# Kernel optimization log

Hardware: AMD Instinct MI355X
Metric: run time of the kernel (lower is better)

The kernel has to match this reference:

```python
import jax, jax.numpy as jnp
import numpy as np

N, M, D = 16384, 16384, 3


def setup_inputs() -> dict:
    key = jax.random.key(0)
    kx, ky = jax.random.split(key)
    x = jax.random.normal(kx, (N, D), dtype=jnp.float32)
    y = jax.random.normal(ky, (M, D), dtype=jnp.float32)
    return {"x": x, "y": y}


def reference(x, y):
    # One-sided Chamfer: for each x_i, min_j ||y_j - x_i||^2.
    x2 = jnp.sum(x * x, axis=-1)                       # [N]
    y2 = jnp.sum(y * y, axis=-1)                       # [M]
    d2 = x2[:, None] - 2.0 * (x @ y.T) + y2[None, :]   # [N, M] pairwise sq dists
    closest_dists = jnp.min(d2, axis=1)                # [N]
    return jnp.sum(closest_dists), closest_dists
```

## Files before the change

### kernel.cpp

```cpp
#include <hip/hip_runtime.h>


constexpr int TPB = 256;
constexpr int XPT = 8;
constexpr int MAX_YCHUNK = 512;

__global__ __launch_bounds__(TPB) void chamfer_main(
    const float* __restrict__ x, const float* __restrict__ y,
    float* __restrict__ part, int N, int M, int ychunk) {
  __shared__ float4 sy[MAX_YCHUNK];
  const int t = threadIdx.x;
  const int bx = blockIdx.x;
  const int s = blockIdx.y;

  for (int jj = t; jj < ychunk; jj += TPB) {
    const int j = s * ychunk + jj;
    if (j < M) {
      const float y0 = y[3 * j], y1 = y[3 * j + 1], y2 = y[3 * j + 2];
      sy[jj] = make_float4(-2.0f * y0, -2.0f * y1, -2.0f * y2,
                           y0 * y0 + y1 * y1 + y2 * y2);
    } else {
      sy[jj] = make_float4(0.0f, 0.0f, 0.0f, __builtin_inff());
    }
  }
  __syncthreads();

  float x0[XPT], x1[XPT], x2[XPT], mn[XPT];
#pragma unroll
  for (int k = 0; k < XPT; k++) {
    const int i = bx * (TPB * XPT) + k * TPB + t;
    const int ic = (i < N) ? i : 0;
    x0[k] = x[3 * ic];
    x1[k] = x[3 * ic + 1];
    x2[k] = x[3 * ic + 2];
    mn[k] = __builtin_inff();
  }

#pragma unroll 4
  for (int jj = 0; jj < ychunk; jj++) {
    const float4 q = sy[jj];
#pragma unroll
    for (int k = 0; k < XPT; k++) {
      mn[k] = fminf(mn[k],
                    fmaf(x0[k], q.x, fmaf(x1[k], q.y, fmaf(x2[k], q.z, q.w))));
    }
  }

#pragma unroll
  for (int k = 0; k < XPT; k++) {
    const int i = bx * (TPB * XPT) + k * TPB + t;
    if (i < N) part[(size_t)s * N + i] = mn[k];
  }
}

__global__ __launch_bounds__(TPB) void chamfer_reduce(
    const float* __restrict__ x, const float* __restrict__ part,
    float* __restrict__ out, int N, int S) {
  const int t = threadIdx.x;
  const int i = blockIdx.x * TPB + t;

  float d = 0.0f;
  if (i < N) {
    float m = __builtin_inff();
#pragma unroll 8
    for (int s = 0; s < S; s++) m = fminf(m, part[(size_t)s * N + i]);
    const float a = x[3 * i], b = x[3 * i + 1], c = x[3 * i + 2];
    d = m + (a * a + b * b + c * c);
    out[1 + i] = d;
  }

  float v = d;
#pragma unroll
  for (int off = 32; off > 0; off >>= 1) v += __shfl_down(v, off, 64);
  __shared__ float wsum[TPB / 64];
  if ((t & 63) == 0) wsum[t >> 6] = v;
  __syncthreads();
  if (t == 0) {
    float s = 0.0f;
#pragma unroll
    for (int w = 0; w < TPB / 64; w++) s += wsum[w];
    atomicAdd(out, s);
  }
}

extern "C" void kernel_launch(void* const* d_in, const int* in_sizes, int n_in,
                              void* d_out, int out_size, void* d_ws, size_t ws_size,
                              hipStream_t stream) {
  const float* x = (const float*)d_in[0];
  const float* y = (const float*)d_in[1];
  float* out = (float*)d_out;

  const int N = in_sizes[0] / 3;
  const int M = in_sizes[1] / 3;

  int S = 64;
  while (S > 8 && (size_t)S * N * sizeof(float) > ws_size) S >>= 1;
  const int ychunk = (M + S - 1) / S;

  float* part = (float*)d_ws;

  hipMemsetAsync(out, 0, sizeof(float), stream);

  const int xblocks = (N + TPB * XPT - 1) / (TPB * XPT);
  dim3 gridB(xblocks, S);
  chamfer_main<<<gridB, TPB, 0, stream>>>(x, y, part, N, M, ychunk);

  const int rblocks = (N + TPB - 1) / TPB;
  chamfer_reduce<<<rblocks, TPB, 0, stream>>>(x, part, out, N, S);
}
```

Before: 86.63 us.

## Process x points in pairs per thread, double y splits, simplify reduction

Each thread now handles 16 x points as float2 pairs, which could let the compiler emit packed FP32 FMA/min instructions. The per-point norm is added in the main kernel, so the reduce kernel no longer reads x. The number of y splits doubles to 128 with a smaller shared chunk, and the reduce kernel uses 64-thread blocks with one atomic per wave. The costs are more partial-result traffic (twice as many rows to reduce), more registers per thread, and fewer x blocks per y split.

```diff
diff --git a/kernel.cpp b/kernel.cpp
--- a/kernel.cpp
+++ b/kernel.cpp
@@ -2,8 +2,8 @@
 
 
 constexpr int TPB = 256;
-constexpr int XPT = 8;
-constexpr int MAX_YCHUNK = 512;
+constexpr int XPAIR = 8;
+constexpr int MAX_YCHUNK = 256;
 
 __global__ __launch_bounds__(TPB) void chamfer_main(
     const float* __restrict__ x, const float* __restrict__ y,
@@ -25,62 +25,66 @@
   }
   __syncthreads();
 
-  float x0[XPT], x1[XPT], x2[XPT], mn[XPT];
+  float2 x0[XPAIR], x1[XPAIR], x2[XPAIR], mn[XPAIR], xsq[XPAIR];
+  const int base = bx * (TPB * 2 * XPAIR) + 2 * t;
 #pragma unroll
-  for (int k = 0; k < XPT; k++) {
-    const int i = bx * (TPB * XPT) + k * TPB + t;
-    const int ic = (i < N) ? i : 0;
-    x0[k] = x[3 * ic];
-    x1[k] = x[3 * ic + 1];
-    x2[k] = x[3 * ic + 2];
-    mn[k] = __builtin_inff();
+  for (int k = 0; k < XPAIR; k++) {
+    int i0 = base + k * 2 * TPB;
+    int i1 = i0 + 1;
+    i0 = (i0 < N) ? i0 : 0;
+    i1 = (i1 < N) ? i1 : 0;
+    x0[k] = make_float2(x[3 * i0], x[3 * i1]);
+    x1[k] = make_float2(x[3 * i0 + 1], x[3 * i1 + 1]);
+    x2[k] = make_float2(x[3 * i0 + 2], x[3 * i1 + 2]);
+    xsq[k].x = x0[k].x * x0[k].x + x1[k].x * x1[k].x + x2[k].x * x2[k].x;
+    xsq[k].y = x0[k].y * x0[k].y + x1[k].y * x1[k].y + x2[k].y * x2[k].y;
+    mn[k] = make_float2(__builtin_inff(), __builtin_inff());
   }
 
-#pragma unroll 4
+#pragma unroll 2
   for (int jj = 0; jj < ychunk; jj++) {
     const float4 q = sy[jj];
 #pragma unroll
-    for (int k = 0; k < XPT; k++) {
-      mn[k] = fminf(mn[k],
-                    fmaf(x0[k], q.x, fmaf(x1[k], q.y, fmaf(x2[k], q.z, q.w))));
+    for (int k = 0; k < XPAIR; k++) {
+      float2 acc;
+      acc.x = fmaf(x2[k].x, q.z, q.w);
+      acc.y = fmaf(x2[k].y, q.z, q.w);
+      acc.x = fmaf(x1[k].x, q.y, acc.x);
+      acc.y = fmaf(x1[k].y, q.y, acc.y);
+      acc.x = fmaf(x0[k].x, q.x, acc.x);
+      acc.y = fmaf(x0[k].y, q.x, acc.y);
+      mn[k].x = fminf(mn[k].x, acc.x);
+      mn[k].y = fminf(mn[k].y, acc.y);
     }
   }
 
+  float2* prow = (float2*)(part + (size_t)s * N);
 #pragma unroll
-  for (int k = 0; k < XPT; k++) {
-    const int i = bx * (TPB * XPT) + k * TPB + t;
-    if (i < N) part[(size_t)s * N + i] = mn[k];
+  for (int k = 0; k < XPAIR; k++) {
+    const int i0 = base + k * 2 * TPB;
+    const float2 v = make_float2(mn[k].x + xsq[k].x, mn[k].y + xsq[k].y);
+    if (i0 + 1 < N) {
+      prow[i0 >> 1] = v;
+    } else if (i0 < N) {
+      part[(size_t)s * N + i0] = v.x;
+    }
   }
 }
 
-__global__ __launch_bounds__(TPB) void chamfer_reduce(
-    const float* __restrict__ x, const float* __restrict__ part,
-    float* __restrict__ out, int N, int S) {
-  const int t = threadIdx.x;
-  const int i = blockIdx.x * TPB + t;
-
-  float d = 0.0f;
+__global__ __launch_bounds__(64) void chamfer_reduce(
+    const float* __restrict__ part, float* __restrict__ out, int N, int S) {
+  const int i = blockIdx.x * 64 + threadIdx.x;
+  float v = 0.0f;
   if (i < N) {
     float m = __builtin_inff();
 #pragma unroll 8
     for (int s = 0; s < S; s++) m = fminf(m, part[(size_t)s * N + i]);
-    const float a = x[3 * i], b = x[3 * i + 1], c = x[3 * i + 2];
-    d = m + (a * a + b * b + c * c);
-    out[1 + i] = d;
+    out[1 + i] = m;
+    v = m;
   }
-
-  float v = d;
 #pragma unroll
   for (int off = 32; off > 0; off >>= 1) v += __shfl_down(v, off, 64);
-  __shared__ float wsum[TPB / 64];
-  if ((t & 63) == 0) wsum[t >> 6] = v;
-  __syncthreads();
-  if (t == 0) {
-    float s = 0.0f;
-#pragma unroll
-    for (int w = 0; w < TPB / 64; w++) s += wsum[w];
-    atomicAdd(out, s);
-  }
+  if (threadIdx.x == 0) atomicAdd(out, v);
 }
 
 extern "C" void kernel_launch(void* const* d_in, const int* in_sizes, int n_in,
@@ -93,7 +97,7 @@
   const int N = in_sizes[0] / 3;
   const int M = in_sizes[1] / 3;
 
-  int S = 64;
+  int S = 128;
   while (S > 8 && (size_t)S * N * sizeof(float) > ws_size) S >>= 1;
   const int ychunk = (M + S - 1) / S;
 
@@ -101,10 +105,10 @@
 
   hipMemsetAsync(out, 0, sizeof(float), stream);
 
-  const int xblocks = (N + TPB * XPT - 1) / (TPB * XPT);
+  const int xblocks = (N + TPB * 2 * XPAIR - 1) / (TPB * 2 * XPAIR);
   dim3 gridB(xblocks, S);
   chamfer_main<<<gridB, TPB, 0, stream>>>(x, y, part, N, M, ychunk);
 
-  const int rblocks = (N + TPB - 1) / TPB;
-  chamfer_reduce<<<rblocks, TPB, 0, stream>>>(x, part, out, N, S);
+  const int rblocks = (N + 63) / 64;
+  chamfer_reduce<<<rblocks, 64, 0, stream>>>(part, out, N, S);
 }
```

Result: slower. 91.51 us (+5.6%).
